# Performance work log

Measured on AMD Instinct MI355X. Metric: run time of the kernel, lower is better.

Reference implementation:

```python
import jax, jax.numpy as jnp
import numpy as np

N_NODES = 50000
N_EDGES = 800000
IN_DIM, HID, EMB = 128, 256, 128


def _gcn_conv(x, src, dst, W, b, n_nodes):
    # PyG GCNConv: add self-loops, symmetric norm D^-1/2 (A+I) D^-1/2, then linear.
    h = x @ W  # [N, out]
    deg = jnp.zeros((n_nodes,), x.dtype).at[dst].add(1.0) + 1.0  # +1 for self-loop
    dinv = jax.lax.rsqrt(deg)
    norm = dinv[src] * dinv[dst]  # [E]
    agg = jnp.zeros_like(h).at[dst].add(h[src] * norm[:, None])
    agg = agg + h * (dinv * dinv)[:, None]  # self-loop term
    return agg + b


def setup_inputs() -> dict:
    key = jax.random.key(0)
    ks = jax.random.split(key, 16)
    s = lambda *sh: None
    x = jax.random.normal(ks[0], (N_NODES, IN_DIM), jnp.float32)
    edge_index = jax.random.randint(ks[1], (2, N_EDGES), 0, N_NODES, jnp.int32)
    def lin(k, fan_in, fan_out):
        lim = 1.0 / np.sqrt(fan_in)
        kw, kb = jax.random.split(k)
        W = jax.random.uniform(kw, (fan_in, fan_out), jnp.float32, -lim, lim)
        b = jax.random.uniform(kb, (fan_out,), jnp.float32, -lim, lim)
        return W, b
    W1, b1 = lin(ks[2], IN_DIM, HID)
    W2, b2 = lin(ks[3], HID, EMB)
    fc1_W, fc1_b = lin(ks[4], EMB, HID)
    fc2_W, fc2_b = lin(ks[5], HID, 1)
    np_W, np_b = lin(ks[6], EMB, 3)
    ep_W, ep_b = lin(ks[7], 2 * EMB, 2)
    gp_W, gp_b = lin(ks[8], EMB, 1)
    return dict(x=x, edge_index=edge_index, W1=W1, b1=b1, W2=W2, b2=b2,
                fc1_W=fc1_W, fc1_b=fc1_b, fc2_W=fc2_W, fc2_b=fc2_b,
                np_W=np_W, np_b=np_b, ep_W=ep_W, ep_b=ep_b, gp_W=gp_W, gp_b=gp_b)


def reference(x, edge_index, W1, b1, W2, b2, fc1_W, fc1_b, fc2_W, fc2_b,
              np_W, np_b, ep_W, ep_b, gp_W, gp_b):
    src, dst = edge_index[0], edge_index[1]
    n = x.shape[0]
    h = jax.nn.relu(_gcn_conv(x, src, dst, W1, b1, n))
    h = jax.nn.relu(_gcn_conv(h, src, dst, W2, b2, n))  # [N, EMB]
    g = jnp.mean(h, axis=0, keepdims=True)  # [1, EMB]
    v = jax.nn.relu(g @ fc1_W + fc1_b)
    value = v @ fc2_W + fc2_b  # [1,1]
    node_logits = h @ np_W + np_b  # [N,3]
    edge_features = jnp.concatenate([h[src], h[dst]], axis=1)  # [E, 2*EMB]
    edge_logits = edge_features @ ep_W + ep_b  # [E,2]
    global_logits = g @ gp_W + gp_b  # [1,1]
    return (node_logits, edge_logits, global_logits, value)
```

## Files before the change

### kernel.cpp

```cpp
#include <hip/hip_runtime.h>
#include <hip/hip_bf16.h>

typedef __attribute__((ext_vector_type(8))) short bf16x8;
typedef __attribute__((ext_vector_type(4))) float f32x4;

__device__ inline unsigned short f2bf(float f) {
    union { float f; unsigned u; } v; v.f = f;
    unsigned r = v.u + 0x7fff + ((v.u >> 16) & 1);
    return (unsigned short)(r >> 16);
}
__device__ inline float bf2f(unsigned short b) {
    union { unsigned u; float f; } v; v.u = ((unsigned)b) << 16;
    return v.f;
}
__device__ inline float bfu_lo(unsigned r) {
    union { unsigned u; float f; } v; v.u = r << 16;
    return v.f;
}
__device__ inline float bfu_hi(unsigned r) {
    union { unsigned u; float f; } v; v.u = r & 0xffff0000u;
    return v.f;
}

__global__ __launch_bounds__(256) void prep_kernel(
    const float* __restrict__ x, unsigned short* __restrict__ xb,
    const float* __restrict__ W1, unsigned short* __restrict__ W1t_hi, unsigned short* __restrict__ W1t_lo,
    const float* __restrict__ W2, unsigned short* __restrict__ W2t_hi, unsigned short* __restrict__ W2t_lo,
    int* __restrict__ zero_ints, float* __restrict__ gsum, int n) {
    int tid = blockIdx.x * blockDim.x + threadIdx.x;
    int C = n * 32;
    if (tid < C) {
        int base = tid * 4;
        float4 v = *(const float4*)&x[base];
        unsigned lo = (unsigned)f2bf(v.x) | ((unsigned)f2bf(v.y) << 16);
        unsigned hi = (unsigned)f2bf(v.z) | ((unsigned)f2bf(v.w) << 16);
        uint2 p; p.x = lo; p.y = hi;
        *(uint2*)&xb[base] = p;
        return;
    }
    tid -= C;
    if (tid < 65536) {
        if (tid < 32768) {
            int k = tid >> 8, j = tid & 255;
            float v = W1[tid];
            unsigned short h = f2bf(v);
            W1t_hi[(size_t)j * 128 + k] = h;
            W1t_lo[(size_t)j * 128 + k] = f2bf(v - bf2f(h));
        } else {
            int i2 = tid - 32768;
            int k = i2 >> 7, j = i2 & 127;
            float v = W2[i2];
            unsigned short h = f2bf(v);
            W2t_hi[(size_t)j * 256 + k] = h;
            W2t_lo[(size_t)j * 256 + k] = f2bf(v - bf2f(h));
        }
        return;
    }
    tid -= 65536;
    if (tid < 3 * n) { zero_ints[tid] = 0; return; }
    tid -= 3 * n;
    if (tid < 128) gsum[tid] = 0.f;
}

__global__ void hist_kernel(const int* __restrict__ dst, int* __restrict__ deg, int nE) {
    int e = blockIdx.x * blockDim.x + threadIdx.x;
    if (e < nE) atomicAdd(&deg[dst[e]], 1);
}

__global__ __launch_bounds__(1024) void scan_kernel(const int* __restrict__ deg,
                                                    int* __restrict__ start,
                                                    float* __restrict__ dinv, int n) {
    __shared__ int wsum[16];
    __shared__ int woff[16];
    __shared__ int carry_s;
    __shared__ int tot_s;
    int t = threadIdx.x, lane = t & 63, wid = t >> 6;
    if (t == 0) carry_s = 0;
    __syncthreads();
    for (int base = 0; base < n; base += 1024) {
        int i = base + t;
        int val = (i < n) ? deg[i] : 0;
        if (i < n) dinv[i] = rsqrtf((float)(val + 1));
        int inc = val;
        for (int s = 1; s < 64; s <<= 1) {
            int tmp = __shfl_up(inc, s);
            if (lane >= s) inc += tmp;
        }
        if (lane == 63) wsum[wid] = inc;
        __syncthreads();
        if (wid == 0) {
            int w = (lane < 16) ? wsum[lane] : 0;
            for (int s = 1; s < 16; s <<= 1) {
                int tmp = __shfl_up(w, s);
                if (lane >= s) w += tmp;
            }
            if (lane < 16) woff[lane] = w - wsum[lane];
            if (lane == 15) tot_s = w;
        }
        __syncthreads();
        if (i < n) start[i] = carry_s + woff[wid] + (inc - val);
        __syncthreads();
        if (t == 0) carry_s += tot_s;
    }
}

__global__ void fill_kernel(const int* __restrict__ src, const int* __restrict__ dst,
                            const int* __restrict__ start, int* __restrict__ cnt,
                            const float* __restrict__ dinv, int2* __restrict__ csr, int nE) {
    int e = blockIdx.x * blockDim.x + threadIdx.x;
    if (e >= nE) return;
    int s = src[e], d = dst[e];
    int pos = start[d] + atomicAdd(&cnt[d], 1);
    float w = dinv[s] * dinv[d];
    csr[pos] = make_int2(s, __float_as_int(w));
}

__global__ __launch_bounds__(256) void gather1_kernel(const unsigned int* __restrict__ xb,
                                                      const int2* __restrict__ csr,
                                                      const int* __restrict__ start,
                                                      const int* __restrict__ deg,
                                                      const float* __restrict__ dinv,
                                                      unsigned int* __restrict__ xin_hi,
                                                      unsigned int* __restrict__ xin_lo, int n) {
    int node = blockIdx.x * 4 + (threadIdx.x >> 6);
    int lane = threadIdx.x & 63;
    if (node >= n) return;
    int p = start[node];
    int e0 = p + deg[node];
    float a0 = 0.f, a1 = 0.f, b0 = 0.f, b1 = 0.f;
    float c0 = 0.f, c1 = 0.f, d0v = 0.f, d1v = 0.f;
    for (; p + 3 < e0; p += 4) {
        int2 q0 = csr[p], q1 = csr[p + 1], q2 = csr[p + 2], q3 = csr[p + 3];
        unsigned r0 = xb[(size_t)q0.x * 64 + lane];
        unsigned r1 = xb[(size_t)q1.x * 64 + lane];
        unsigned r2 = xb[(size_t)q2.x * 64 + lane];
        unsigned r3 = xb[(size_t)q3.x * 64 + lane];
        float w0 = __int_as_float(q0.y), w1 = __int_as_float(q1.y);
        float w2 = __int_as_float(q2.y), w3 = __int_as_float(q3.y);
        a0 += w0 * bfu_lo(r0); a1 += w0 * bfu_hi(r0);
        b0 += w1 * bfu_lo(r1); b1 += w1 * bfu_hi(r1);
        c0 += w2 * bfu_lo(r2); c1 += w2 * bfu_hi(r2);
        d0v += w3 * bfu_lo(r3); d1v += w3 * bfu_hi(r3);
    }
    for (; p < e0; ++p) {
        int2 q = csr[p];
        float w = __int_as_float(q.y);
        unsigned r = xb[(size_t)q.x * 64 + lane];
        a0 += w * bfu_lo(r); a1 += w * bfu_hi(r);
    }
    a0 = (a0 + b0) + (c0 + d0v);
    a1 = (a1 + b1) + (c1 + d1v);
    float di = dinv[node];
    float d2 = di * di;
    unsigned rs = xb[(size_t)node * 64 + lane];
    a0 += d2 * bfu_lo(rs);
    a1 += d2 * bfu_hi(rs);
    unsigned short h0 = f2bf(a0), h1 = f2bf(a1);
    xin_hi[(size_t)node * 64 + lane] = (unsigned)h0 | ((unsigned)h1 << 16);
    unsigned short l0 = f2bf(a0 - bf2f(h0)), l1 = f2bf(a1 - bf2f(h1));
    xin_lo[(size_t)node * 64 + lane] = (unsigned)l0 | ((unsigned)l1 << 16);
}

template <int K, int NOUT, bool BIAS_RELU_SPLIT>
__global__ __launch_bounds__(256) void mfma_gemm_kernel(
    const unsigned short* __restrict__ Ahi, const unsigned short* __restrict__ Alo,
    const unsigned short* __restrict__ Wthi, const unsigned short* __restrict__ Wtlo,
    const float* __restrict__ bias,
    unsigned short* __restrict__ Ohi, unsigned short* __restrict__ Olo, int n) {
    int w = threadIdx.x >> 6, l = threadIdx.x & 63;
    int m0 = blockIdx.x * 128 + w * 32;
    int j0 = blockIdx.y * 64;
    int col16 = l & 15;
    int koff = (l >> 4) * 8;
    int rowA0 = m0 + col16;       if (rowA0 >= n) rowA0 = n - 1;
    int rowA1 = m0 + 16 + col16;  if (rowA1 >= n) rowA1 = n - 1;
    f32x4 acc[2][4];
#pragma unroll
    for (int g = 0; g < 2; ++g)
#pragma unroll
        for (int c = 0; c < 4; ++c) acc[g][c] = (f32x4){0.f, 0.f, 0.f, 0.f};
    for (int k0 = 0; k0 < K; k0 += 32) {
        bf16x8 ah0 = *(const bf16x8*)&Ahi[(size_t)rowA0 * K + k0 + koff];
        bf16x8 al0 = *(const bf16x8*)&Alo[(size_t)rowA0 * K + k0 + koff];
        bf16x8 ah1 = *(const bf16x8*)&Ahi[(size_t)rowA1 * K + k0 + koff];
        bf16x8 al1 = *(const bf16x8*)&Alo[(size_t)rowA1 * K + k0 + koff];
#pragma unroll
        for (int c = 0; c < 4; ++c) {
            size_t wb = (size_t)(j0 + c * 16 + col16) * K + k0 + koff;
            bf16x8 wh = *(const bf16x8*)&Wthi[wb];
            bf16x8 wl = *(const bf16x8*)&Wtlo[wb];
            acc[0][c] = __builtin_amdgcn_mfma_f32_16x16x32_bf16(ah0, wh, acc[0][c], 0, 0, 0);
            acc[0][c] = __builtin_amdgcn_mfma_f32_16x16x32_bf16(al0, wh, acc[0][c], 0, 0, 0);
            acc[0][c] = __builtin_amdgcn_mfma_f32_16x16x32_bf16(ah0, wl, acc[0][c], 0, 0, 0);
            acc[1][c] = __builtin_amdgcn_mfma_f32_16x16x32_bf16(ah1, wh, acc[1][c], 0, 0, 0);
            acc[1][c] = __builtin_amdgcn_mfma_f32_16x16x32_bf16(al1, wh, acc[1][c], 0, 0, 0);
            acc[1][c] = __builtin_amdgcn_mfma_f32_16x16x32_bf16(ah1, wl, acc[1][c], 0, 0, 0);
        }
    }
#pragma unroll
    for (int g = 0; g < 2; ++g) {
#pragma unroll
        for (int c = 0; c < 4; ++c) {
            int col = j0 + c * 16 + col16;
#pragma unroll
            for (int r = 0; r < 4; ++r) {
                int orow = m0 + g * 16 + (l >> 4) * 4 + r;
                if (orow >= n) continue;
                float v = acc[g][c][r];
                if (BIAS_RELU_SPLIT) {
                    v = fmaxf(v + bias[col], 0.f);
                    unsigned short hb = f2bf(v);
                    Ohi[(size_t)orow * NOUT + col] = hb;
                    Olo[(size_t)orow * NOUT + col] = f2bf(v - bf2f(hb));
                } else {
                    Ohi[(size_t)orow * NOUT + col] = f2bf(v);
                }
            }
        }
    }
}

__global__ __launch_bounds__(256) void conv2_fused_kernel(
    const unsigned int* __restrict__ h2b, const int2* __restrict__ csr,
    const int* __restrict__ start, const int* __restrict__ deg,
    const float* __restrict__ dinv, const float* __restrict__ b2,
    const float* __restrict__ npW, const float* __restrict__ npb,
    const float* __restrict__ epW, const float* __restrict__ epb,
    float* __restrict__ out_nl, float* __restrict__ uv,
    float* __restrict__ gsum, int n) {
    __shared__ float lgs[4][128];
    int lane = threadIdx.x & 63;
    int wid = threadIdx.x >> 6;
    int d0 = lane * 2, d1 = lane * 2 + 1;
    float wn00 = npW[d0 * 3 + 0], wn10 = npW[d0 * 3 + 1], wn20 = npW[d0 * 3 + 2];
    float wn01 = npW[d1 * 3 + 0], wn11 = npW[d1 * 3 + 1], wn21 = npW[d1 * 3 + 2];
    float wu00 = epW[d0 * 2 + 0], wu10 = epW[d0 * 2 + 1];
    float wu01 = epW[d1 * 2 + 0], wu11 = epW[d1 * 2 + 1];
    float wv00 = epW[(d0 + 128) * 2 + 0], wv10 = epW[(d0 + 128) * 2 + 1];
    float wv01 = epW[(d1 + 128) * 2 + 0], wv11 = epW[(d1 + 128) * 2 + 1];
    float b20 = b2[d0], b21 = b2[d1];
    float npb0 = npb[0], npb1 = npb[1], npb2 = npb[2];
    float epb0 = epb[0], epb1 = epb[1];
    float p0 = 0.f, p1 = 0.f;

    for (int node = blockIdx.x * 4 + wid; node < n; node += gridDim.x * 4) {
        int p = start[node];
        int e0 = p + deg[node];
        float a0 = 0.f, a1 = 0.f, b0 = 0.f, b1 = 0.f;
        float c0 = 0.f, c1 = 0.f, e0v = 0.f, e1v = 0.f;
        for (; p + 3 < e0; p += 4) {
            int2 q0 = csr[p], q1 = csr[p + 1], q2 = csr[p + 2], q3 = csr[p + 3];
            unsigned r0 = h2b[(size_t)q0.x * 64 + lane];
            unsigned r1 = h2b[(size_t)q1.x * 64 + lane];
            unsigned r2 = h2b[(size_t)q2.x * 64 + lane];
            unsigned r3 = h2b[(size_t)q3.x * 64 + lane];
            float w0 = __int_as_float(q0.y), w1 = __int_as_float(q1.y);
            float w2 = __int_as_float(q2.y), w3 = __int_as_float(q3.y);
            a0 += w0 * bfu_lo(r0); a1 += w0 * bfu_hi(r0);
            b0 += w1 * bfu_lo(r1); b1 += w1 * bfu_hi(r1);
            c0 += w2 * bfu_lo(r2); c1 += w2 * bfu_hi(r2);
            e0v += w3 * bfu_lo(r3); e1v += w3 * bfu_hi(r3);
        }
        for (; p < e0; ++p) {
            int2 q = csr[p];
            float w = __int_as_float(q.y);
            unsigned r = h2b[(size_t)q.x * 64 + lane];
            a0 += w * bfu_lo(r); a1 += w * bfu_hi(r);
        }
        a0 = (a0 + b0) + (c0 + e0v);
        a1 = (a1 + b1) + (c1 + e1v);
        float di = dinv[node];
        float d2 = di * di;
        unsigned rs = h2b[(size_t)node * 64 + lane];
        a0 = fmaxf(a0 + d2 * bfu_lo(rs) + b20, 0.f);
        a1 = fmaxf(a1 + d2 * bfu_hi(rs) + b21, 0.f);
        p0 += a0;
        p1 += a1;
        float n0 = a0 * wn00 + a1 * wn01;
        float n1 = a0 * wn10 + a1 * wn11;
        float n2 = a0 * wn20 + a1 * wn21;
        float u0 = a0 * wu00 + a1 * wu01;
        float u1 = a0 * wu10 + a1 * wu11;
        float v0 = a0 * wv00 + a1 * wv01;
        float v1 = a0 * wv10 + a1 * wv11;
        for (int off = 32; off; off >>= 1) {
            n0 += __shfl_xor(n0, off);
            n1 += __shfl_xor(n1, off);
            n2 += __shfl_xor(n2, off);
            u0 += __shfl_xor(u0, off);
            u1 += __shfl_xor(u1, off);
            v0 += __shfl_xor(v0, off);
            v1 += __shfl_xor(v1, off);
        }
        if (lane == 0) {
            out_nl[(size_t)node * 3 + 0] = n0 + npb0;
            out_nl[(size_t)node * 3 + 1] = n1 + npb1;
            out_nl[(size_t)node * 3 + 2] = n2 + npb2;
            float4 o;
            o.x = u0 + epb0; o.y = u1 + epb1; o.z = v0; o.w = v1;
            *(float4*)&uv[(size_t)node * 4] = o;
        }
    }
    lgs[wid][d0] = p0;
    lgs[wid][d1] = p1;
    __syncthreads();
    int t = threadIdx.x;
    if (t < 128) {
        float tot = lgs[0][t] + lgs[1][t] + lgs[2][t] + lgs[3][t];
        atomicAdd(&gsum[t], tot);
    }
}

__global__ void head_kernel(const float* __restrict__ gsum,
                            const float* __restrict__ fc1W, const float* __restrict__ fc1b,
                            const float* __restrict__ fc2W, const float* __restrict__ fc2b,
                            const float* __restrict__ gpW, const float* __restrict__ gpb,
                            float* __restrict__ out_gl, float* __restrict__ out_val, int n) {
    __shared__ float g[128];
    __shared__ float red[256];
    int t = threadIdx.x;
    if (t < 128) g[t] = gsum[t] * (1.0f / (float)n);
    __syncthreads();
    float v = fc1b[t];
#pragma unroll
    for (int k = 0; k < 128; ++k) v += g[k] * fc1W[k * 256 + t];
    v = fmaxf(v, 0.0f);
    red[t] = v * fc2W[t];
    __syncthreads();
    for (int s = 128; s > 0; s >>= 1) { if (t < s) red[t] += red[t + s]; __syncthreads(); }
    if (t == 0) out_val[0] = red[0] + fc2b[0];
    __syncthreads();
    red[t] = (t < 128) ? g[t] * gpW[t] : 0.0f;
    __syncthreads();
    for (int s = 128; s > 0; s >>= 1) { if (t < s) red[t] += red[t + s]; __syncthreads(); }
    if (t == 0) out_gl[0] = red[0] + gpb[0];
}

__global__ void edge_kernel(const float* __restrict__ uv, const int* __restrict__ src,
                            const int* __restrict__ dst, float* __restrict__ out, int nE) {
    int e = blockIdx.x * blockDim.x + threadIdx.x;
    if (e >= nE) return;
    int s = src[e], d = dst[e];
    float2 u = *(const float2*)&uv[(size_t)s * 4];
    float2 v = *(const float2*)&uv[(size_t)d * 4 + 2];
    float2 o; o.x = u.x + v.x; o.y = u.y + v.y;
    *(float2*)&out[(size_t)e * 2] = o;
}

extern "C" void kernel_launch(void* const* d_in, const int* in_sizes, int n_in,
                              void* d_out, int out_size, void* d_ws, size_t ws_size,
                              hipStream_t stream) {
    const float* x    = (const float*)d_in[0];
    const int*   ei   = (const int*)d_in[1];
    const float* W1   = (const float*)d_in[2];
    const float* b1   = (const float*)d_in[3];
    const float* W2   = (const float*)d_in[4];
    const float* b2   = (const float*)d_in[5];
    const float* fc1W = (const float*)d_in[6];
    const float* fc1b = (const float*)d_in[7];
    const float* fc2W = (const float*)d_in[8];
    const float* fc2b = (const float*)d_in[9];
    const float* npW  = (const float*)d_in[10];
    const float* npb  = (const float*)d_in[11];
    const float* epW  = (const float*)d_in[12];
    const float* epb  = (const float*)d_in[13];
    const float* gpW  = (const float*)d_in[14];
    const float* gpb  = (const float*)d_in[15];
    float* out = (float*)d_out;

    const int n = in_sizes[0] / 128;
    const int E = in_sizes[1] / 2;
    const int* src = ei;
    const int* dst = ei + E;

    char* p = (char*)d_ws;
    auto alloc = [&](size_t bytes) { char* r = p; p += (bytes + 255) & ~(size_t)255; return r; };
    unsigned short* xb     = (unsigned short*)alloc((size_t)n * 128 * 2);
    unsigned short* xin_hi = (unsigned short*)alloc((size_t)n * 128 * 2);
    unsigned short* xin_lo = (unsigned short*)alloc((size_t)n * 128 * 2);
    unsigned short* h_hi   = (unsigned short*)alloc((size_t)n * 256 * 2);
    unsigned short* h_lo   = (unsigned short*)alloc((size_t)n * 256 * 2);
    unsigned short* W1t_hi = (unsigned short*)alloc(128 * 256 * 2);
    unsigned short* W1t_lo = (unsigned short*)alloc(128 * 256 * 2);
    unsigned short* W2t_hi = (unsigned short*)alloc(256 * 128 * 2);
    unsigned short* W2t_lo = (unsigned short*)alloc(256 * 128 * 2);
    int2*  csr    = (int2*)alloc((size_t)E * 8);
    int*   deg    = (int*)alloc((size_t)n * 4 * 3);
    int*   startp = deg + n;
    int*   cnt    = startp + n;
    float* dinv   = (float*)alloc((size_t)n * 4);
    float* uv     = (float*)alloc((size_t)n * 16);
    float* gsum   = (float*)alloc(512);
    unsigned short* h2b = xb;

    float* out_nl  = out;
    float* out_el  = out + (size_t)n * 3;
    float* out_gl  = out + (size_t)n * 3 + (size_t)E * 2;
    float* out_val = out_gl + 1;

    {
        long total = (long)n * 32 + 65536 + 3L * n + 128;
        int blocks = (int)((total + 255) / 256);
        prep_kernel<<<blocks, 256, 0, stream>>>(x, xb, W1, W1t_hi, W1t_lo,
                                                W2, W2t_hi, W2t_lo, deg, gsum, n);
    }

    hist_kernel<<<(E + 255) / 256, 256, 0, stream>>>(dst, deg, E);
    scan_kernel<<<1, 1024, 0, stream>>>(deg, startp, dinv, n);
    fill_kernel<<<(E + 255) / 256, 256, 0, stream>>>(src, dst, startp, cnt, dinv, csr, E);

    gather1_kernel<<<(n + 3) / 4, 256, 0, stream>>>((const unsigned int*)xb, csr, startp, deg,
                                                    dinv, (unsigned int*)xin_hi,
                                                    (unsigned int*)xin_lo, n);

    dim3 g1((n + 127) / 128, 256 / 64);
    mfma_gemm_kernel<128, 256, true><<<g1, 256, 0, stream>>>(xin_hi, xin_lo, W1t_hi, W1t_lo,
                                                             b1, h_hi, h_lo, n);
    dim3 g2((n + 127) / 128, 128 / 64);
    mfma_gemm_kernel<256, 128, false><<<g2, 256, 0, stream>>>(h_hi, h_lo, W2t_hi, W2t_lo,
                                                              nullptr, h2b, nullptr, n);

    conv2_fused_kernel<<<2048, 256, 0, stream>>>((const unsigned int*)h2b, csr, startp, deg,
                                                 dinv, b2, npW, npb, epW, epb,
                                                 out_nl, uv, gsum, n);

    head_kernel<<<1, 256, 0, stream>>>(gsum, fc1W, fc1b, fc2W, fc2b, gpW, gpb, out_gl, out_val, n);
    edge_kernel<<<(E + 255) / 256, 256, 0, stream>>>(uv, src, dst, out_el, E);
}
```

Measured before the change: 480.8 us.

## Parallelize degree scan, unroll gathers by 8, drop hidden lo split, fuse head+edge

Replaces the single-block serial prefix scan with a two-level multi-block scan (per-block local offsets plus a block-offset array), and updates consumers to add the block offset. Gather loops in both conv stages are unrolled to 8 edges with the self-row load hoisted, to increase memory-level parallelism. The layer-1 hidden output is stored as a single bf16 instead of hi/lo pairs, removing one buffer write and a third of the MFMAs in the second GEMM at some precision cost. The head and edge kernels are merged into one launch.

Result: faster. 407.1 us (-15.3%).

```diff
diff --git a/kernel.cpp b/kernel.cpp
--- a/kernel.cpp
+++ b/kernel.cpp
@@ -57,8 +57,8 @@
         return;
     }
     tid -= 65536;
-    if (tid < 3 * n) { zero_ints[tid] = 0; return; }
-    tid -= 3 * n;
+    if (tid < 2 * n) { zero_ints[tid] = 0; return; }
+    tid -= 2 * n;
     if (tid < 128) gsum[tid] = 0.f;
 }
 
@@ -67,57 +67,63 @@
     if (e < nE) atomicAdd(&deg[dst[e]], 1);
 }
 
-__global__ __launch_bounds__(1024) void scan_kernel(const int* __restrict__ deg,
-                                                    int* __restrict__ start,
-                                                    float* __restrict__ dinv, int n) {
+__global__ __launch_bounds__(1024) void scanA_kernel(const int* __restrict__ deg,
+                                                     int* __restrict__ local,
+                                                     float* __restrict__ dinv,
+                                                     int* __restrict__ bsum, int n) {
     __shared__ int wsum[16];
     __shared__ int woff[16];
-    __shared__ int carry_s;
-    __shared__ int tot_s;
     int t = threadIdx.x, lane = t & 63, wid = t >> 6;
-    if (t == 0) carry_s = 0;
+    int i = blockIdx.x * 1024 + t;
+    int val = (i < n) ? deg[i] : 0;
+    if (i < n) dinv[i] = rsqrtf((float)(val + 1));
+    int inc = val;
+    for (int s = 1; s < 64; s <<= 1) {
+        int tmp = __shfl_up(inc, s);
+        if (lane >= s) inc += tmp;
+    }
+    if (lane == 63) wsum[wid] = inc;
     __syncthreads();
-    for (int base = 0; base < n; base += 1024) {
-        int i = base + t;
-        int val = (i < n) ? deg[i] : 0;
-        if (i < n) dinv[i] = rsqrtf((float)(val + 1));
-        int inc = val;
-        for (int s = 1; s < 64; s <<= 1) {
-            int tmp = __shfl_up(inc, s);
-            if (lane >= s) inc += tmp;
-        }
-        if (lane == 63) wsum[wid] = inc;
-        __syncthreads();
-        if (wid == 0) {
-            int w = (lane < 16) ? wsum[lane] : 0;
-            for (int s = 1; s < 16; s <<= 1) {
-                int tmp = __shfl_up(w, s);
-                if (lane >= s) w += tmp;
-            }
-            if (lane < 16) woff[lane] = w - wsum[lane];
-            if (lane == 15) tot_s = w;
-        }
-        __syncthreads();
-        if (i < n) start[i] = carry_s + woff[wid] + (inc - val);
-        __syncthreads();
-        if (t == 0) carry_s += tot_s;
-    }
+    if (wid == 0) {
+        int w = (lane < 16) ? wsum[lane] : 0;
+        for (int s = 1; s < 16; s <<= 1) {
+            int tmp = __shfl_up(w, s);
+            if (lane >= s) w += tmp;
+        }
+        if (lane < 16) woff[lane] = w - wsum[lane];
+        if (lane == 15) bsum[blockIdx.x] = w;
+    }
+    __syncthreads();
+    if (i < n) local[i] = woff[wid] + (inc - val);
+}
+
+__global__ void scanB_kernel(const int* __restrict__ bsum, int* __restrict__ boff, int nb) {
+    int lane = threadIdx.x & 63;
+    int v = (lane < nb) ? bsum[lane] : 0;
+    int inc = v;
+    for (int s = 1; s < 64; s <<= 1) {
+        int tmp = __shfl_up(inc, s);
+        if (lane >= s) inc += tmp;
+    }
+    if (lane < nb) boff[lane] = inc - v;
 }
 
 __global__ void fill_kernel(const int* __restrict__ src, const int* __restrict__ dst,
-                            const int* __restrict__ start, int* __restrict__ cnt,
-                            const float* __restrict__ dinv, int2* __restrict__ csr, int nE) {
+                            const int* __restrict__ local, const int* __restrict__ boff,
+                            int* __restrict__ cnt, const float* __restrict__ dinv,
+                            int2* __restrict__ csr, int nE) {
     int e = blockIdx.x * blockDim.x + threadIdx.x;
     if (e >= nE) return;
     int s = src[e], d = dst[e];
-    int pos = start[d] + atomicAdd(&cnt[d], 1);
+    int pos = local[d] + boff[d >> 10] + atomicAdd(&cnt[d], 1);
     float w = dinv[s] * dinv[d];
     csr[pos] = make_int2(s, __float_as_int(w));
 }
 
 __global__ __launch_bounds__(256) void gather1_kernel(const unsigned int* __restrict__ xb,
                                                       const int2* __restrict__ csr,
-                                                      const int* __restrict__ start,
+                                                      const int* __restrict__ local,
+                                                      const int* __restrict__ boff,
                                                       const int* __restrict__ deg,
                                                       const float* __restrict__ dinv,
                                                       unsigned int* __restrict__ xin_hi,
@@ -125,10 +131,35 @@
     int node = blockIdx.x * 4 + (threadIdx.x >> 6);
     int lane = threadIdx.x & 63;
     if (node >= n) return;
-    int p = start[node];
+    int p = local[node] + boff[node >> 10];
     int e0 = p + deg[node];
+    unsigned rs = xb[(size_t)node * 64 + lane];
     float a0 = 0.f, a1 = 0.f, b0 = 0.f, b1 = 0.f;
     float c0 = 0.f, c1 = 0.f, d0v = 0.f, d1v = 0.f;
+    for (; p + 7 < e0; p += 8) {
+        int2 q0 = csr[p], q1 = csr[p + 1], q2 = csr[p + 2], q3 = csr[p + 3];
+        int2 q4 = csr[p + 4], q5 = csr[p + 5], q6 = csr[p + 6], q7 = csr[p + 7];
+        unsigned r0 = xb[(size_t)q0.x * 64 + lane];
+        unsigned r1 = xb[(size_t)q1.x * 64 + lane];
+        unsigned r2 = xb[(size_t)q2.x * 64 + lane];
+        unsigned r3 = xb[(size_t)q3.x * 64 + lane];
+        unsigned r4 = xb[(size_t)q4.x * 64 + lane];
+        unsigned r5 = xb[(size_t)q5.x * 64 + lane];
+        unsigned r6 = xb[(size_t)q6.x * 64 + lane];
+        unsigned r7 = xb[(size_t)q7.x * 64 + lane];
+        float w0 = __int_as_float(q0.y), w1 = __int_as_float(q1.y);
+        float w2 = __int_as_float(q2.y), w3 = __int_as_float(q3.y);
+        float w4 = __int_as_float(q4.y), w5 = __int_as_float(q5.y);
+        float w6 = __int_as_float(q6.y), w7 = __int_as_float(q7.y);
+        a0 += w0 * bfu_lo(r0); a1 += w0 * bfu_hi(r0);
+        b0 += w1 * bfu_lo(r1); b1 += w1 * bfu_hi(r1);
+        c0 += w2 * bfu_lo(r2); c1 += w2 * bfu_hi(r2);
+        d0v += w3 * bfu_lo(r3); d1v += w3 * bfu_hi(r3);
+        a0 += w4 * bfu_lo(r4); a1 += w4 * bfu_hi(r4);
+        b0 += w5 * bfu_lo(r5); b1 += w5 * bfu_hi(r5);
+        c0 += w6 * bfu_lo(r6); c1 += w6 * bfu_hi(r6);
+        d0v += w7 * bfu_lo(r7); d1v += w7 * bfu_hi(r7);
+    }
     for (; p + 3 < e0; p += 4) {
         int2 q0 = csr[p], q1 = csr[p + 1], q2 = csr[p + 2], q3 = csr[p + 3];
         unsigned r0 = xb[(size_t)q0.x * 64 + lane];
@@ -152,7 +183,6 @@
     a1 = (a1 + b1) + (c1 + d1v);
     float di = dinv[node];
     float d2 = di * di;
-    unsigned rs = xb[(size_t)node * 64 + lane];
     a0 += d2 * bfu_lo(rs);
     a1 += d2 * bfu_hi(rs);
     unsigned short h0 = f2bf(a0), h1 = f2bf(a1);
@@ -161,12 +191,12 @@
     xin_lo[(size_t)node * 64 + lane] = (unsigned)l0 | ((unsigned)l1 << 16);
 }
 
-template <int K, int NOUT, bool BIAS_RELU_SPLIT>
+template <int K, int NOUT, bool BIAS_RELU, bool A_SPLIT>
 __global__ __launch_bounds__(256) void mfma_gemm_kernel(
     const unsigned short* __restrict__ Ahi, const unsigned short* __restrict__ Alo,
     const unsigned short* __restrict__ Wthi, const unsigned short* __restrict__ Wtlo,
     const float* __restrict__ bias,
-    unsigned short* __restrict__ Ohi, unsigned short* __restrict__ Olo, int n) {
+    unsigned short* __restrict__ O, int n) {
     int w = threadIdx.x >> 6, l = threadIdx.x & 63;
     int m0 = blockIdx.x * 128 + w * 32;
     int j0 = blockIdx.y * 64;
@@ -181,19 +211,22 @@
         for (int c = 0; c < 4; ++c) acc[g][c] = (f32x4){0.f, 0.f, 0.f, 0.f};
     for (int k0 = 0; k0 < K; k0 += 32) {
         bf16x8 ah0 = *(const bf16x8*)&Ahi[(size_t)rowA0 * K + k0 + koff];
-        bf16x8 al0 = *(const bf16x8*)&Alo[(size_t)rowA0 * K + k0 + koff];
         bf16x8 ah1 = *(const bf16x8*)&Ahi[(size_t)rowA1 * K + k0 + koff];
-        bf16x8 al1 = *(const bf16x8*)&Alo[(size_t)rowA1 * K + k0 + koff];
+        bf16x8 al0, al1;
+        if (A_SPLIT) {
+            al0 = *(const bf16x8*)&Alo[(size_t)rowA0 * K + k0 + koff];
+            al1 = *(const bf16x8*)&Alo[(size_t)rowA1 * K + k0 + koff];
+        }
 #pragma unroll
         for (int c = 0; c < 4; ++c) {
             size_t wb = (size_t)(j0 + c * 16 + col16) * K + k0 + koff;
             bf16x8 wh = *(const bf16x8*)&Wthi[wb];
             bf16x8 wl = *(const bf16x8*)&Wtlo[wb];
             acc[0][c] = __builtin_amdgcn_mfma_f32_16x16x32_bf16(ah0, wh, acc[0][c], 0, 0, 0);
-            acc[0][c] = __builtin_amdgcn_mfma_f32_16x16x32_bf16(al0, wh, acc[0][c], 0, 0, 0);
+            if (A_SPLIT) acc[0][c] = __builtin_amdgcn_mfma_f32_16x16x32_bf16(al0, wh, acc[0][c], 0, 0, 0);
             acc[0][c] = __builtin_amdgcn_mfma_f32_16x16x32_bf16(ah0, wl, acc[0][c], 0, 0, 0);
             acc[1][c] = __builtin_amdgcn_mfma_f32_16x16x32_bf16(ah1, wh, acc[1][c], 0, 0, 0);
-            acc[1][c] = __builtin_amdgcn_mfma_f32_16x16x32_bf16(al1, wh, acc[1][c], 0, 0, 0);
+            if (A_SPLIT) acc[1][c] = __builtin_amdgcn_mfma_f32_16x16x32_bf16(al1, wh, acc[1][c], 0, 0, 0);
             acc[1][c] = __builtin_amdgcn_mfma_f32_16x16x32_bf16(ah1, wl, acc[1][c], 0, 0, 0);
         }
     }
@@ -207,14 +240,8 @@
                 int orow = m0 + g * 16 + (l >> 4) * 4 + r;
                 if (orow >= n) continue;
                 float v = acc[g][c][r];
-                if (BIAS_RELU_SPLIT) {
-                    v = fmaxf(v + bias[col], 0.f);
-                    unsigned short hb = f2bf(v);
-                    Ohi[(size_t)orow * NOUT + col] = hb;
-                    Olo[(size_t)orow * NOUT + col] = f2bf(v - bf2f(hb));
-                } else {
-                    Ohi[(size_t)orow * NOUT + col] = f2bf(v);
-                }
+                if (BIAS_RELU) v = fmaxf(v + bias[col], 0.f);
+                O[(size_t)orow * NOUT + col] = f2bf(v);
             }
         }
     }
@@ -222,7 +249,8 @@
 
 __global__ __launch_bounds__(256) void conv2_fused_kernel(
     const unsigned int* __restrict__ h2b, const int2* __restrict__ csr,
-    const int* __restrict__ start, const int* __restrict__ deg,
+    const int* __restrict__ local, const int* __restrict__ boff,
+    const int* __restrict__ deg,
     const float* __restrict__ dinv, const float* __restrict__ b2,
     const float* __restrict__ npW, const float* __restrict__ npb,
     const float* __restrict__ epW, const float* __restrict__ epb,
@@ -244,10 +272,35 @@
     float p0 = 0.f, p1 = 0.f;
 
     for (int node = blockIdx.x * 4 + wid; node < n; node += gridDim.x * 4) {
-        int p = start[node];
+        int p = local[node] + boff[node >> 10];
         int e0 = p + deg[node];
+        unsigned rs = h2b[(size_t)node * 64 + lane];
         float a0 = 0.f, a1 = 0.f, b0 = 0.f, b1 = 0.f;
         float c0 = 0.f, c1 = 0.f, e0v = 0.f, e1v = 0.f;
+        for (; p + 7 < e0; p += 8) {
+            int2 q0 = csr[p], q1 = csr[p + 1], q2 = csr[p + 2], q3 = csr[p + 3];
+            int2 q4 = csr[p + 4], q5 = csr[p + 5], q6 = csr[p + 6], q7 = csr[p + 7];
+            unsigned r0 = h2b[(size_t)q0.x * 64 + lane];
+            unsigned r1 = h2b[(size_t)q1.x * 64 + lane];
+            unsigned r2 = h2b[(size_t)q2.x * 64 + lane];
+            unsigned r3 = h2b[(size_t)q3.x * 64 + lane];
+            unsigned r4 = h2b[(size_t)q4.x * 64 + lane];
+            unsigned r5 = h2b[(size_t)q5.x * 64 + lane];
+            unsigned r6 = h2b[(size_t)q6.x * 64 + lane];
+            unsigned r7 = h2b[(size_t)q7.x * 64 + lane];
+            float w0 = __int_as_float(q0.y), w1 = __int_as_float(q1.y);
+            float w2 = __int_as_float(q2.y), w3 = __int_as_float(q3.y);
+            float w4 = __int_as_float(q4.y), w5 = __int_as_float(q5.y);
+            float w6 = __int_as_float(q6.y), w7 = __int_as_float(q7.y);
+            a0 += w0 * bfu_lo(r0); a1 += w0 * bfu_hi(r0);
+            b0 += w1 * bfu_lo(r1); b1 += w1 * bfu_hi(r1);
+            c0 += w2 * bfu_lo(r2); c1 += w2 * bfu_hi(r2);
+            e0v += w3 * bfu_lo(r3); e1v += w3 * bfu_hi(r3);
+            a0 += w4 * bfu_lo(r4); a1 += w4 * bfu_hi(r4);
+            b0 += w5 * bfu_lo(r5); b1 += w5 * bfu_hi(r5);
+            c0 += w6 * bfu_lo(r6); c1 += w6 * bfu_hi(r6);
+            e0v += w7 * bfu_lo(r7); e1v += w7 * bfu_hi(r7);
+        }
         for (; p + 3 < e0; p += 4) {
             int2 q0 = csr[p], q1 = csr[p + 1], q2 = csr[p + 2], q3 = csr[p + 3];
             unsigned r0 = h2b[(size_t)q0.x * 64 + lane];
@@ -271,7 +324,6 @@
         a1 = (a1 + b1) + (c1 + e1v);
         float di = dinv[node];
         float d2 = di * di;
-        unsigned rs = h2b[(size_t)node * 64 + lane];
         a0 = fmaxf(a0 + d2 * bfu_lo(rs) + b20, 0.f);
         a1 = fmaxf(a1 + d2 * bfu_hi(rs) + b21, 0.f);
         p0 += a0;
@@ -311,40 +363,42 @@
     }
 }
 
-__global__ void head_kernel(const float* __restrict__ gsum,
-                            const float* __restrict__ fc1W, const float* __restrict__ fc1b,
-                            const float* __restrict__ fc2W, const float* __restrict__ fc2b,
-                            const float* __restrict__ gpW, const float* __restrict__ gpb,
-                            float* __restrict__ out_gl, float* __restrict__ out_val, int n) {
-    __shared__ float g[128];
-    __shared__ float red[256];
-    int t = threadIdx.x;
-    if (t < 128) g[t] = gsum[t] * (1.0f / (float)n);
-    __syncthreads();
-    float v = fc1b[t];
-#pragma unroll
-    for (int k = 0; k < 128; ++k) v += g[k] * fc1W[k * 256 + t];
-    v = fmaxf(v, 0.0f);
-    red[t] = v * fc2W[t];
-    __syncthreads();
-    for (int s = 128; s > 0; s >>= 1) { if (t < s) red[t] += red[t + s]; __syncthreads(); }
-    if (t == 0) out_val[0] = red[0] + fc2b[0];
-    __syncthreads();
-    red[t] = (t < 128) ? g[t] * gpW[t] : 0.0f;
-    __syncthreads();
-    for (int s = 128; s > 0; s >>= 1) { if (t < s) red[t] += red[t + s]; __syncthreads(); }
-    if (t == 0) out_gl[0] = red[0] + gpb[0];
-}
-
-__global__ void edge_kernel(const float* __restrict__ uv, const int* __restrict__ src,
-                            const int* __restrict__ dst, float* __restrict__ out, int nE) {
-    int e = blockIdx.x * blockDim.x + threadIdx.x;
+__global__ __launch_bounds__(256) void edge_head_kernel(
+    const float* __restrict__ uv, const int* __restrict__ src, const int* __restrict__ dst,
+    float* __restrict__ out_el, int nE,
+    const float* __restrict__ gsum,
+    const float* __restrict__ fc1W, const float* __restrict__ fc1b,
+    const float* __restrict__ fc2W, const float* __restrict__ fc2b,
+    const float* __restrict__ gpW, const float* __restrict__ gpb,
+    float* __restrict__ out_gl, float* __restrict__ out_val, int n) {
+    if (blockIdx.x == 0) {
+        __shared__ float g[128];
+        __shared__ float red[256];
+        int t = threadIdx.x;
+        if (t < 128) g[t] = gsum[t] * (1.0f / (float)n);
+        __syncthreads();
+        float v = fc1b[t];
+#pragma unroll
+        for (int k = 0; k < 128; ++k) v += g[k] * fc1W[k * 256 + t];
+        v = fmaxf(v, 0.0f);
+        red[t] = v * fc2W[t];
+        __syncthreads();
+        for (int s = 128; s > 0; s >>= 1) { if (t < s) red[t] += red[t + s]; __syncthreads(); }
+        if (t == 0) out_val[0] = red[0] + fc2b[0];
+        __syncthreads();
+        red[t] = (t < 128) ? g[t] * gpW[t] : 0.0f;
+        __syncthreads();
+        for (int s = 128; s > 0; s >>= 1) { if (t < s) red[t] += red[t + s]; __syncthreads(); }
+        if (t == 0) out_gl[0] = red[0] + gpb[0];
+        return;
+    }
+    int e = (blockIdx.x - 1) * blockDim.x + threadIdx.x;
     if (e >= nE) return;
     int s = src[e], d = dst[e];
     float2 u = *(const float2*)&uv[(size_t)s * 4];
     float2 v = *(const float2*)&uv[(size_t)d * 4 + 2];
     float2 o; o.x = u.x + v.x; o.y = u.y + v.y;
-    *(float2*)&out[(size_t)e * 2] = o;
+    *(float2*)&out_el[(size_t)e * 2] = o;
 }
 
 extern "C" void kernel_launch(void* const* d_in, const int* in_sizes, int n_in,
@@ -372,22 +426,24 @@
     const int E = in_sizes[1] / 2;
     const int* src = ei;
     const int* dst = ei + E;
+    const int nb = (n + 1023) / 1024;
 
     char* p = (char*)d_ws;
     auto alloc = [&](size_t bytes) { char* r = p; p += (bytes + 255) & ~(size_t)255; return r; };
     unsigned short* xb     = (unsigned short*)alloc((size_t)n * 128 * 2);
     unsigned short* xin_hi = (unsigned short*)alloc((size_t)n * 128 * 2);
     unsigned short* xin_lo = (unsigned short*)alloc((size_t)n * 128 * 2);
-    unsigned short* h_hi   = (unsigned short*)alloc((size_t)n * 256 * 2);
-    unsigned short* h_lo   = (unsigned short*)alloc((size_t)n * 256 * 2);
+    unsigned short* h      = (unsigned short*)alloc((size_t)n * 256 * 2);
     unsigned short* W1t_hi = (unsigned short*)alloc(128 * 256 * 2);
     unsigned short* W1t_lo = (unsigned short*)alloc(128 * 256 * 2);
     unsigned short* W2t_hi = (unsigned short*)alloc(256 * 128 * 2);
     unsigned short* W2t_lo = (unsigned short*)alloc(256 * 128 * 2);
     int2*  csr    = (int2*)alloc((size_t)E * 8);
-    int*   deg    = (int*)alloc((size_t)n * 4 * 3);
-    int*   startp = deg + n;
-    int*   cnt    = startp + n;
+    int*   deg    = (int*)alloc((size_t)n * 4 * 2);
+    int*   cnt    = deg + n;
+    int*   local  = (int*)alloc((size_t)n * 4);
+    int*   bsum   = (int*)alloc(64 * 4);
+    int*   boff   = (int*)alloc(64 * 4);
     float* dinv   = (float*)alloc((size_t)n * 4);
     float* uv     = (float*)alloc((size_t)n * 16);
     float* gsum   = (float*)alloc(512);
@@ -399,31 +455,33 @@
     float* out_val = out_gl + 1;
 
     {
-        long total = (long)n * 32 + 65536 + 3L * n + 128;
+        long total = (long)n * 32 + 65536 + 2L * n + 128;
         int blocks = (int)((total + 255) / 256);
         prep_kernel<<<blocks, 256, 0, stream>>>(x, xb, W1, W1t_hi, W1t_lo,
                                                 W2, W2t_hi, W2t_lo, deg, gsum, n);
     }
 
     hist_kernel<<<(E + 255) / 256, 256, 0, stream>>>(dst, deg, E);
-    scan_kernel<<<1, 1024, 0, stream>>>(deg, startp, dinv, n);
-    fill_kernel<<<(E + 255) / 256, 256, 0, stream>>>(src, dst, startp, cnt, dinv, csr, E);
-
-    gather1_kernel<<<(n + 3) / 4, 256, 0, stream>>>((const unsigned int*)xb, csr, startp, deg,
-                                                    dinv, (unsigned int*)xin_hi,
+    scanA_kernel<<<nb, 1024, 0, stream>>>(deg, local, dinv, bsum, n);
+    scanB_kernel<<<1, 64, 0, stream>>>(bsum, boff, nb);
+    fill_kernel<<<(E + 255) / 256, 256, 0, stream>>>(src, dst, local, boff, cnt, dinv, csr, E);
+
+    gather1_kernel<<<(n + 3) / 4, 256, 0, stream>>>((const unsigned int*)xb, csr, local, boff,
+                                                    deg, dinv, (unsigned int*)xin_hi,
                                                     (unsigned int*)xin_lo, n);
 
     dim3 g1((n + 127) / 128, 256 / 64);
-    mfma_gemm_kernel<128, 256, true><<<g1, 256, 0, stream>>>(xin_hi, xin_lo, W1t_hi, W1t_lo,
-                                                             b1, h_hi, h_lo, n);
+    mfma_gemm_kernel<128, 256, true, true><<<g1, 256, 0, stream>>>(xin_hi, xin_lo, W1t_hi, W1t_lo,
+                                                                   b1, h, n);
     dim3 g2((n + 127) / 128, 128 / 64);
-    mfma_gemm_kernel<256, 128, false><<<g2, 256, 0, stream>>>(h_hi, h_lo, W2t_hi, W2t_lo,
-                                                              nullptr, h2b, nullptr, n);
-
-    conv2_fused_kernel<<<2048, 256, 0, stream>>>((const unsigned int*)h2b, csr, startp, deg,
-                                                 dinv, b2, npW, npb, epW, epb,
+    mfma_gemm_kernel<256, 128, false, false><<<g2, 256, 0, stream>>>(h, nullptr, W2t_hi, W2t_lo,
+                                                                     nullptr, h2b, n);
+
+    conv2_fused_kernel<<<2048, 256, 0, stream>>>((const unsigned int*)h2b, csr, local, boff,
+                                                 deg, dinv, b2, npW, npb, epW, epb,
                                                  out_nl, uv, gsum, n);
 
-    head_kernel<<<1, 256, 0, stream>>>(gsum, fc1W, fc1b, fc2W, fc2b, gpW, gpb, out_gl, out_val, n);
-    edge_kernel<<<(E + 255) / 256, 256, 0, stream>>>(uv, src, dst, out_el, E);
-}
+    edge_head_kernel<<<1 + (E + 255) / 256, 256, 0, stream>>>(uv, src, dst, out_el, E,
+                                                              gsum, fc1W, fc1b, fc2W, fc2b,
+                                                              gpW, gpb, out_gl, out_val, n);
+}
```
